# Performance work log

Measured on AMD Instinct MI355X. Metric: run time of the kernel, lower is better.

Reference implementation:

```python
import jax, jax.numpy as jnp
import numpy as np

L, B, D, Di, N, H, P, K, M, V = 4, 8, 2048, 4096, 128, 64, 64, 4, 8, 50288
Cch = Di + 2 * N           # conv channels = 4352
Dout = 2 * Di + 2 * N + H  # in_proj out = 8512
EPS = 1e-5


def _rms(x, w):
    return x * jax.lax.rsqrt(jnp.mean(x * x, axis=-1, keepdims=True) + EPS) * w


def setup_inputs() -> dict:
    key = jax.random.key(0)
    ks = jax.random.split(key, 16)
    s = 0.02
    return {
        "input_ids": jax.random.randint(ks[0], (B, 1), 0, V),
        "emb": jax.random.normal(ks[1], (V, D)) * s,
        "in_proj_w": jax.random.normal(ks[2], (L, D, Dout)) * s,
        "conv_w": jax.random.normal(ks[3], (L, Cch, K)) * s,
        "conv_b": jax.random.normal(ks[4], (L, Cch)) * s,
        "A_log": jax.random.normal(ks[5], (L, H)) * 0.5,
        "dt_bias": jax.random.normal(ks[6], (L, H)) * 0.5,
        "D_param": jax.random.normal(ks[7], (L, H)) * 0.5,
        "mixer_norm_w": jnp.ones((L, Di)),
        "out_proj_w": jax.random.normal(ks[8], (L, Di, D)) * s,
        "layer_norm_w": jnp.ones((L, D)),
        "norm_f_w": jnp.ones((D,)),
        "W_mc": jax.random.normal(ks[9], (L, M + 1)).at[:, -1].set(5.0),
        "conv_state": jax.random.normal(ks[10], (L, B, Cch, K)) * 0.1,
        "ssm_state": jax.random.normal(ks[11], (L, B, H, P, N)) * 0.1,
        "cached_states": jax.random.normal(ks[12], (L, B, M, H, P, N)) * 0.1,
    }


def reference(input_ids, emb, in_proj_w, conv_w, conv_b, A_log, dt_bias, D_param,
              mixer_norm_w, out_proj_w, layer_norm_w, norm_f_w, W_mc,
              conv_state, ssm_state, cached_states):
    ids = input_ids[:, 0]              # (B,)
    res = emb[ids]                     # (B, D) token embedding gather
    for l in range(L):
        xn = _rms(res, layer_norm_w[l])
        zxbcdt = xn @ in_proj_w[l]     # (B, Dout)
        z = zxbcdt[:, :Di]
        xBC = zxbcdt[:, Di:Di + Cch]
        dt = zxbcdt[:, Di + Cch:]
        # circular conv-state shift + depthwise conv over kernel dim
        cs = jnp.concatenate([conv_state[l][:, :, 1:], xBC[:, :, None]], axis=-1)
        xBC = jax.nn.silu(jnp.sum(cs * conv_w[l][None], axis=-1) + conv_b[l])
        x, Bm, Cm = xBC[:, :Di], xBC[:, Di:Di + N], xBC[:, Di + N:]
        dt = jax.nn.softplus(dt + dt_bias[l])                 # (B, H)
        dA = jnp.exp(dt * (-jnp.exp(A_log[l])))               # (B, H)
        x = x.reshape(B, H, P)
        dBx = jnp.einsum('bh,bn,bhp->bhpn', dt, Bm, x)        # (B,H,P,N)
        ssm = ssm_state[l] * dA[:, :, None, None] + dBx       # (B,H,P,N)
        # softmax-weighted fusion of cached segment states + current state
        w = jax.nn.softmax(W_mc[l])                           # (M+1,)
        fused = jnp.einsum('bmhpn,m->bhpn', cached_states[l], w[:-1]) + w[-1] * ssm
        y = jnp.einsum('bhpn,bn->bhp', fused, Cm) + D_param[l][None, :, None] * x
        y = y.reshape(B, Di)
        y = _rms(y * jax.nn.silu(z), mixer_norm_w[l])         # gated RMSNorm
        res = res + y @ out_proj_w[l]
    res = _rms(res, norm_f_w)
    logits = res @ emb.T               # tied lm_head
    return logits[:, None, :]          # (B, 1, V)
```

## Files before the change

### kernel.cpp

```cpp
#include <hip/hip_runtime.h>
#include <hip/hip_bf16.h>
#include <math.h>

#define LN 4
#define B_ 8
#define D_ 2048
#define DI 4096
#define N_ 128
#define H_ 64
#define P_ 64
#define K_ 4
#define M_ 8
#define V_ 50288
#define CCH (DI + 2*N_)
#define DOUT (2*DI + 2*N_ + H_)
#define EPSF 1e-5f
#define KT_IN 32
#define KT_OUT 128
#define SSQS 16

typedef float f32x4 __attribute__((ext_vector_type(4)));

__device__ inline float wave_sum(float v) {
  #pragma unroll
  for (int off = 32; off > 0; off >>= 1) v += __shfl_xor(v, off, 64);
  return v;
}

__device__ inline float fold_reduce8(const float a[8], int lane) {
  float t0[4];
  #pragma unroll
  for (int r = 0; r < 4; ++r) {
    float keep = (lane & 1) ? a[2*r+1] : a[2*r];
    float send = (lane & 1) ? a[2*r]   : a[2*r+1];
    t0[r] = keep + __shfl_xor(send, 1, 64);
  }
  float t1[2];
  #pragma unroll
  for (int r = 0; r < 2; ++r) {
    float keep = (lane & 2) ? t0[2*r+1] : t0[2*r];
    float send = (lane & 2) ? t0[2*r]   : t0[2*r+1];
    t1[r] = keep + __shfl_xor(send, 2, 64);
  }
  float keep = (lane & 4) ? t1[1] : t1[0];
  float send = (lane & 4) ? t1[0] : t1[1];
  float u = keep + __shfl_xor(send, 4, 64);
  u += __shfl_xor(u, 8, 64);
  u += __shfl_xor(u, 16, 64);
  u += __shfl_xor(u, 32, 64);
  return u;
}

__global__ __launch_bounds__(256)
void k_inproj1_first(const int* __restrict__ ids, const float* __restrict__ emb,
                     const float* __restrict__ lnw, const float* __restrict__ W,
                     float* __restrict__ pin) {
  __shared__ float xs[8][64];
  __shared__ float sred[4][8];
  int tid = threadIdx.x, lane = tid & 63, wid = tid >> 6;
  int jt = blockIdx.x % 9, kt = blockIdx.x / 9;
  int k0 = kt * 64;
  float ssq[8];
  #pragma unroll
  for (int r = 0; r < 8; ++r) {
    const float* row = emb + (size_t)ids[r] * D_;
    f32x4 a = *reinterpret_cast<const f32x4*>(row + tid * 8);
    f32x4 c = *reinterpret_cast<const f32x4*>(row + tid * 8 + 4);
    ssq[r] = a[0]*a[0] + a[1]*a[1] + a[2]*a[2] + a[3]*a[3]
           + c[0]*c[0] + c[1]*c[1] + c[2]*c[2] + c[3]*c[3];
  }
  #pragma unroll
  for (int r = 0; r < 8; ++r) {
    float wsum = wave_sum(ssq[r]);
    if (lane == 0) sred[wid][r] = wsum;
  }
  __syncthreads();
  for (int i = tid; i < 8 * 64; i += 256) {
    int r = i >> 6, kk = i & 63;
    const float* row = emb + (size_t)ids[r] * D_;
    float tot = sred[0][r] + sred[1][r] + sred[2][r] + sred[3][r];
    float scale = rsqrtf(tot / (float)D_ + EPSF);
    xs[r][kk] = row[k0 + kk] * scale * lnw[k0 + kk];
  }
  __syncthreads();
  int j = jt * 1024 + tid * 4;
  if (j >= DOUT) return;
  f32x4 acc[8];
  #pragma unroll
  for (int r = 0; r < 8; ++r) acc[r] = (f32x4)0.f;
  const float* Wp = W + (size_t)k0 * DOUT + j;
  for (int kk = 0; kk < 64; ++kk) {
    f32x4 w4 = __builtin_nontemporal_load(
        reinterpret_cast<const f32x4*>(Wp + (size_t)kk * DOUT));
    #pragma unroll
    for (int r = 0; r < 8; ++r) acc[r] += w4 * xs[r][kk];
  }
  #pragma unroll
  for (int r = 0; r < 8; ++r)
    *reinterpret_cast<f32x4*>(&pin[((size_t)kt * 8 + r) * DOUT + j]) = acc[r];
}

__global__ __launch_bounds__(256)
void k_inproj1(const float* __restrict__ res, const float* __restrict__ ssq_in,
               const float* __restrict__ lnw, const float* __restrict__ W,
               float* __restrict__ pin) {
  __shared__ float xs[8][64];
  int tid = threadIdx.x;
  int jt = blockIdx.x % 9, kt = blockIdx.x / 9;
  int k0 = kt * 64;
  for (int i = tid; i < 8 * 64; i += 256) {
    int r = i >> 6, kk = i & 63;
    float scale = rsqrtf(ssq_in[r * SSQS] / (float)D_ + EPSF);
    xs[r][kk] = res[r * D_ + k0 + kk] * scale * lnw[k0 + kk];
  }
  __syncthreads();
  int j = jt * 1024 + tid * 4;
  if (j >= DOUT) return;
  f32x4 acc[8];
  #pragma unroll
  for (int r = 0; r < 8; ++r) acc[r] = (f32x4)0.f;
  const float* Wp = W + (size_t)k0 * DOUT + j;
  for (int kk = 0; kk < 64; ++kk) {
    f32x4 w4 = __builtin_nontemporal_load(
        reinterpret_cast<const f32x4*>(Wp + (size_t)kk * DOUT));
    #pragma unroll
    for (int r = 0; r < 8; ++r) acc[r] += w4 * xs[r][kk];
  }
  #pragma unroll
  for (int r = 0; r < 8; ++r)
    *reinterpret_cast<f32x4*>(&pin[((size_t)kt * 8 + r) * DOUT + j]) = acc[r];
}

__global__ __launch_bounds__(256)
void k_inproj2_conv(const float* __restrict__ pin, const float* __restrict__ conv_state,
                    const float* __restrict__ conv_w, const float* __restrict__ conv_b,
                    const float* __restrict__ A_log, const float* __restrict__ dt_bias,
                    const float* __restrict__ W_mc,
                    float* __restrict__ zx, float* __restrict__ xbc,
                    float* __restrict__ dts, float* __restrict__ dav,
                    float* __restrict__ wmc) {
  __shared__ f32x4 red[4][64];
  const int TOT4 = B_ * DOUT / 4;
  int tid = threadIdx.x;
  int el = tid & 63, kq = tid >> 6;
  int e = blockIdx.x * 64 + el;
  f32x4 s = (f32x4)0.f;
  const f32x4* p4 = reinterpret_cast<const f32x4*>(pin) + e;
  #pragma unroll
  for (int kk = 0; kk < 8; ++kk)
    s += p4[(size_t)(kq * 8 + kk) * TOT4];
  red[kq][el] = s;
  __syncthreads();
  if (tid >= 64) return;
  s = red[0][tid] + red[1][tid] + red[2][tid] + red[3][tid];
  reinterpret_cast<f32x4*>(zx)[e] = s;
  int c4 = e * 4;
  int b = c4 / DOUT;
  int c = c4 - b * DOUT;
  #pragma unroll
  for (int q = 0; q < 4; ++q) {
    int ce = c + q;
    if (ce >= DI && ce < DI + CCH) {
      int cc = ce - DI;
      f32x4 cs4 = *reinterpret_cast<const f32x4*>(conv_state + ((size_t)b * CCH + cc) * K_);
      f32x4 cw4 = *reinterpret_cast<const f32x4*>(conv_w + (size_t)cc * K_);
      float v = cs4[1] * cw4[0] + cs4[2] * cw4[1] + cs4[3] * cw4[2]
              + s[q] * cw4[3] + conv_b[cc];
      xbc[b * CCH + cc] = v / (1.f + expf(-v));
    } else if (ce >= DI + CCH) {
      int h = ce - DI - CCH;
      float x = s[q] + dt_bias[h];
      float sp = (x > 20.f) ? x : log1pf(expf(x));
      dts[b * 64 + h] = sp;
      dav[b * 64 + h] = expf(-expf(A_log[h]) * sp);
    }
  }
  if (blockIdx.x == 0 && tid == 0) {
    float mx = -1e30f;
    for (int i = 0; i < M_ + 1; ++i) mx = fmaxf(mx, W_mc[i]);
    float e2[M_ + 1], sum = 0.f;
    for (int i = 0; i < M_ + 1; ++i) { e2[i] = expf(W_mc[i] - mx); sum += e2[i]; }
    for (int i = 0; i < M_ + 1; ++i) wmc[i] = e2[i] / sum;
  }
}

__global__ __launch_bounds__(256)
void k_state(const float* __restrict__ xbc, const float* __restrict__ dts,
             const float* __restrict__ dav, const float* __restrict__ Dp_,
             const float* __restrict__ wmc, const float* __restrict__ ssm,
             const float* __restrict__ cached, float* __restrict__ y) {
  int wg = blockIdx.x * 4 + (threadIdx.x >> 6);
  int lane = threadIdx.x & 63;
  int b = wg >> 11;
  int h = (wg >> 5) & 63;
  int pp = wg & 31;
  int hf = lane >> 5, il = lane & 31;
  int p = pp * 2 + hf;
  float xv  = xbc[b * CCH + h * 64 + p];
  float dtv = dts[b * 64 + h];
  float da  = dav[b * 64 + h];
  float w8  = wmc[8];
  const f32x4* xb4 = reinterpret_cast<const f32x4*>(xbc);
  f32x4 B4 = xb4[b * (CCH / 4) + DI / 4 + il];
  f32x4 C4 = xb4[b * (CCH / 4) + DI / 4 + N_ / 4 + il];
  const f32x4* sp4 = reinterpret_cast<const f32x4*>(ssm) +
                     ((size_t)((b * H_ + h) * P_ + p)) * (N_ / 4) + il;
  const f32x4* cp4 = reinterpret_cast<const f32x4*>(cached) +
                     ((size_t)(((b * M_) * H_ + h) * P_ + p)) * (N_ / 4) + il;
  f32x4 s4 = __builtin_nontemporal_load(sp4);
  f32x4 f4 = (s4 * da + B4 * (dtv * xv)) * w8;
  #pragma unroll
  for (int m = 0; m < 8; ++m) {
    f32x4 c4 = __builtin_nontemporal_load(cp4 + (size_t)m * (H_ * P_ * N_ / 4));
    f4 += c4 * wmc[m];
  }
  f4 *= C4;
  float acc = f4[0] + f4[1] + f4[2] + f4[3];
  #pragma unroll
  for (int off = 1; off < 32; off <<= 1) acc += __shfl_xor(acc, off, 64);
  if (il == 0) y[b * DI + h * 64 + p] = acc + Dp_[h] * xv;
}

__global__ __launch_bounds__(1024)
void k_gatednorm(const float* __restrict__ y, const float* __restrict__ zx,
                 const float* __restrict__ mnw, float* __restrict__ yg,
                 float* __restrict__ ssq_in) {
  __shared__ float lds[16];
  int b = blockIdx.x, tid = threadIdx.x;
  if (tid < 8) ssq_in[tid * SSQS] = 0.f;
  float tv[4];
  float ss = 0.f;
  #pragma unroll
  for (int t = 0; t < 4; ++t) {
    int i = tid + t * 1024;
    float z = zx[b * DOUT + i];
    float v = y[b * DI + i] * (z / (1.f + expf(-z)));
    tv[t] = v; ss += v * v;
  }
  float wsum = wave_sum(ss);
  int lane = tid & 63, wid = tid >> 6;
  if (lane == 0) lds[wid] = wsum;
  __syncthreads();
  float tot = 0.f;
  #pragma unroll
  for (int i = 0; i < 16; ++i) tot += lds[i];
  float scale = rsqrtf(tot / (float)DI + EPSF);
  #pragma unroll
  for (int t = 0; t < 4; ++t) {
    int i = tid + t * 1024;
    yg[b * DI + i] = tv[t] * scale * mnw[i];
  }
}

__global__ void k_outproj1(const float* __restrict__ yg, const float* __restrict__ W,
                           float* __restrict__ pout) {
  __shared__ float xs[8][32];
  int jt = blockIdx.x & 1, kt = blockIdx.x >> 1;
  int k0 = kt * 32;
  for (int i = threadIdx.x; i < 8 * 32; i += 256) {
    int r = i >> 5, kk = i & 31;
    xs[r][kk] = yg[r * DI + k0 + kk];
  }
  __syncthreads();
  int j = jt * 1024 + threadIdx.x * 4;
  f32x4 acc[8];
  #pragma unroll
  for (int r = 0; r < 8; ++r) acc[r] = (f32x4)0.f;
  const float* Wp = W + (size_t)k0 * D_ + j;
  for (int kk = 0; kk < 32; ++kk) {
    f32x4 w4 = __builtin_nontemporal_load(
        reinterpret_cast<const f32x4*>(Wp + (size_t)kk * D_));
    #pragma unroll
    for (int r = 0; r < 8; ++r) acc[r] += w4 * xs[r][kk];
  }
  #pragma unroll
  for (int r = 0; r < 8; ++r)
    *reinterpret_cast<f32x4*>(&pout[((size_t)kt * 8 + r) * D_ + j]) = acc[r];
}

__global__ __launch_bounds__(256)
void k_outproj2(const float* __restrict__ pout, float* __restrict__ res,
                const int* __restrict__ ids, const float* __restrict__ emb,
                float* __restrict__ ssq_in) {
  __shared__ f32x4 red[16][16];
  const int TOT4 = B_ * D_ / 4;
  int tid = threadIdx.x;
  int pl = tid & 15, kq = tid >> 4;
  int pos = blockIdx.x * 16 + pl;
  const f32x4* p4 = reinterpret_cast<const f32x4*>(pout) + pos;
  f32x4 s = (f32x4)0.f;
  #pragma unroll
  for (int kk = 0; kk < 8; ++kk)
    s += p4[(size_t)(kq * 8 + kk) * TOT4];
  red[pl][kq] = s;
  __syncthreads();
  if (tid < 16) {
    f32x4 tot = (f32x4)0.f;
    #pragma unroll
    for (int q = 0; q < 16; ++q) tot += red[tid][q];
    int mypos = blockIdx.x * 16 + tid;
    f32x4* r4 = reinterpret_cast<f32x4*>(res);
    f32x4 nv;
    if (ids) {
      int b = mypos >> 9, d4 = mypos & 511;
      f32x4 base = reinterpret_cast<const f32x4*>(emb)[(size_t)ids[b] * (D_ / 4) + d4];
      nv = base + tot;
    } else {
      nv = r4[mypos] + tot;
    }
    r4[mypos] = nv;
    float ps = nv[0]*nv[0] + nv[1]*nv[1] + nv[2]*nv[2] + nv[3]*nv[3];
    #pragma unroll
    for (int off = 1; off < 16; off <<= 1) ps += __shfl_xor(ps, off, 64);
    if (tid == 0) atomicAdd(&ssq_in[(mypos >> 9) * SSQS], ps);
  }
}

#define SL_ 4
#define KS_ (D_ / SL_)
#define NVB16 (V_ / 16)
__global__ __launch_bounds__(256)
void k_logits(const float* __restrict__ res, const float* __restrict__ ssq_in,
              const float* __restrict__ nfw, const float* __restrict__ emb,
              float* __restrict__ pl) {
  __shared__ f32x4 xs[8][KS_ / 4];
  int s = blockIdx.x & 3, vb = blockIdx.x >> 2;
  const f32x4* res4 = reinterpret_cast<const f32x4*>(res);
  const f32x4* nfw4 = reinterpret_cast<const f32x4*>(nfw);
  for (int i = threadIdx.x; i < 8 * (KS_ / 4); i += 256) {
    int r = i >> 7, q = i & 127;
    float scale = rsqrtf(ssq_in[r * SSQS] / (float)D_ + EPSF);
    xs[r][q] = res4[r * (D_ / 4) + s * (KS_ / 4) + q] * scale
             * nfw4[s * (KS_ / 4) + q];
  }
  __syncthreads();
  int wid = threadIdx.x >> 6, lane = threadIdx.x & 63;
  int v0 = vb * 16 + wid * 4;
  const f32x4* e4 = reinterpret_cast<const f32x4*>(emb);
  #pragma unroll
  for (int vv = 0; vv < 4; ++vv) {
    int v = v0 + vv;
    const f32x4* ep = e4 + (size_t)v * (D_ / 4) + s * (KS_ / 4);
    float acc[8] = {0,0,0,0,0,0,0,0};
    #pragma unroll
    for (int st = 0; st < KS_ / 256; ++st) {
      int c = st * 64 + lane;
      f32x4 e = __builtin_nontemporal_load(ep + c);
      #pragma unroll
      for (int r = 0; r < 8; ++r) {
        f32x4 x = xs[r][c];
        acc[r] += e[0]*x[0] + e[1]*x[1] + e[2]*x[2] + e[3]*x[3];
      }
    }
    float u = fold_reduce8(acc, lane);
    if (lane < 8) pl[((size_t)s * 8 + lane) * V_ + v] = u;
  }
}

__global__ __launch_bounds__(256)
void k_logits2(const float* __restrict__ pl, float* __restrict__ out) {
  int v = blockIdx.x * 256 + threadIdx.x;
  if (v >= V_) return;
  int r = blockIdx.y;
  float t = pl[(size_t)r * V_ + v]
          + pl[((size_t)8  + r) * V_ + v]
          + pl[((size_t)16 + r) * V_ + v]
          + pl[((size_t)24 + r) * V_ + v];
  out[(size_t)r * V_ + v] = t;
}

extern "C" void kernel_launch(void* const* d_in, const int* in_sizes, int n_in,
                              void* d_out, int out_size, void* d_ws, size_t ws_size,
                              hipStream_t stream) {
  const int*   ids    = (const int*)  d_in[0];
  const float* emb    = (const float*)d_in[1];
  const float* inW    = (const float*)d_in[2];
  const float* convW  = (const float*)d_in[3];
  const float* convB  = (const float*)d_in[4];
  const float* Alog   = (const float*)d_in[5];
  const float* dtB    = (const float*)d_in[6];
  const float* Dpar   = (const float*)d_in[7];
  const float* mnw    = (const float*)d_in[8];
  const float* outW   = (const float*)d_in[9];
  const float* lnw    = (const float*)d_in[10];
  const float* nfw    = (const float*)d_in[11];
  const float* Wmc    = (const float*)d_in[12];
  const float* convS  = (const float*)d_in[13];
  const float* ssmS   = (const float*)d_in[14];
  const float* cached = (const float*)d_in[15];
  float* out = (float*)d_out;
  float* ws  = (float*)d_ws;

  float* res   = ws;
  float* zx    = ws + 16384;
  float* xbc   = ws + 84480;
  float* dts   = ws + 119296;
  float* dav   = ws + 119808;
  float* wmc   = ws + 120320;
  float* ssqi  = ws + 120384;
  float* y     = ws + 120512;
  float* yg    = ws + 153280;
  float* pin   = ws + 186048;
  float* pout  = ws + 2365120;
  float* pl    = ws + 4462272;

  for (int l = 0; l < LN; ++l) {
    if (l == 0)
      k_inproj1_first<<<288, 256, 0, stream>>>(ids, emb, lnw, inW, pin);
    else
      k_inproj1<<<288, 256, 0, stream>>>(res, ssqi, lnw + (size_t)l * D_,
                                         inW + (size_t)l * D_ * DOUT, pin);
    k_inproj2_conv<<<266, 256, 0, stream>>>(pin,
        convS + (size_t)l * B_ * CCH * K_, convW + (size_t)l * CCH * K_,
        convB + (size_t)l * CCH, Alog + l * H_, dtB + l * H_, Wmc + l * (M_ + 1),
        zx, xbc, dts, dav, wmc);
    k_state<<<4096, 256, 0, stream>>>(xbc, dts, dav, Dpar + l * H_, wmc,
        ssmS + (size_t)l * B_ * H_ * P_ * N_,
        cached + (size_t)l * B_ * M_ * H_ * P_ * N_, y);
    k_gatednorm<<<8, 1024, 0, stream>>>(y, zx, mnw + (size_t)l * DI, yg, ssqi);
    k_outproj1<<<256, 256, 0, stream>>>(yg, outW + (size_t)l * DI * D_, pout);
    k_outproj2<<<256, 256, 0, stream>>>(pout, res,
                                        (l == 0) ? ids : nullptr, emb, ssqi);
  }
  k_logits<<<NVB16 * SL_, 256, 0, stream>>>(res, ssqi, nfw, emb, pl);
  k_logits2<<<dim3((V_ + 255) / 256, 8), 256, 0, stream>>>(pl, out);
}
```

Measured before the change: 418.6 us.

## Fuse gated RMSNorm into state and out-projection kernels, drop gatednorm launch

Removes the separate k_gatednorm kernel (8 blocks of 1024 threads) by having k_state emit per-block partial sums of the squared gated output, and having k_outproj1 reduce those partials and apply the gate, scale and norm weight while staging its input tile. The ssq_in zeroing moves into k_inproj2_conv. This saves one launch and a low-parallelism kernel per layer. In exchange, every out-projection block re-reduces 4096 partials and recomputes the silu gate, and k_state gains a block-level syncthreads.

```diff
diff --git a/kernel.cpp b/kernel.cpp
--- a/kernel.cpp
+++ b/kernel.cpp
@@ -138,10 +138,11 @@
                     const float* __restrict__ W_mc,
                     float* __restrict__ zx, float* __restrict__ xbc,
                     float* __restrict__ dts, float* __restrict__ dav,
-                    float* __restrict__ wmc) {
+                    float* __restrict__ wmc, float* __restrict__ ssq_in) {
   __shared__ f32x4 red[4][64];
   const int TOT4 = B_ * DOUT / 4;
   int tid = threadIdx.x;
+  if (blockIdx.x == 1 && tid < 8) ssq_in[tid * SSQS] = 0.f;
   int el = tid & 63, kq = tid >> 6;
   int e = blockIdx.x * 64 + el;
   f32x4 s = (f32x4)0.f;
@@ -185,10 +186,12 @@
 }
 
 __global__ __launch_bounds__(256)
-void k_state(const float* __restrict__ xbc, const float* __restrict__ dts,
-             const float* __restrict__ dav, const float* __restrict__ Dp_,
-             const float* __restrict__ wmc, const float* __restrict__ ssm,
-             const float* __restrict__ cached, float* __restrict__ y) {
+void k_state(const float* __restrict__ xbc, const float* __restrict__ zx,
+             const float* __restrict__ dts, const float* __restrict__ dav,
+             const float* __restrict__ Dp_, const float* __restrict__ wmc,
+             const float* __restrict__ ssm, const float* __restrict__ cached,
+             float* __restrict__ y, float* __restrict__ gpart) {
+  __shared__ float gred[8];
   int wg = blockIdx.x * 4 + (threadIdx.x >> 6);
   int lane = threadIdx.x & 63;
   int b = wg >> 11;
@@ -218,51 +221,49 @@
   float acc = f4[0] + f4[1] + f4[2] + f4[3];
   #pragma unroll
   for (int off = 1; off < 32; off <<= 1) acc += __shfl_xor(acc, off, 64);
-  if (il == 0) y[b * DI + h * 64 + p] = acc + Dp_[h] * xv;
-}
-
-__global__ __launch_bounds__(1024)
-void k_gatednorm(const float* __restrict__ y, const float* __restrict__ zx,
-                 const float* __restrict__ mnw, float* __restrict__ yg,
-                 float* __restrict__ ssq_in) {
-  __shared__ float lds[16];
-  int b = blockIdx.x, tid = threadIdx.x;
-  if (tid < 8) ssq_in[tid * SSQS] = 0.f;
-  float tv[4];
-  float ss = 0.f;
-  #pragma unroll
-  for (int t = 0; t < 4; ++t) {
-    int i = tid + t * 1024;
-    float z = zx[b * DOUT + i];
-    float v = y[b * DI + i] * (z / (1.f + expf(-z)));
-    tv[t] = v; ss += v * v;
-  }
-  float wsum = wave_sum(ss);
-  int lane = tid & 63, wid = tid >> 6;
-  if (lane == 0) lds[wid] = wsum;
-  __syncthreads();
-  float tot = 0.f;
-  #pragma unroll
-  for (int i = 0; i < 16; ++i) tot += lds[i];
-  float scale = rsqrtf(tot / (float)DI + EPSF);
-  #pragma unroll
-  for (int t = 0; t < 4; ++t) {
-    int i = tid + t * 1024;
-    yg[b * DI + i] = tv[t] * scale * mnw[i];
-  }
-}
-
-__global__ void k_outproj1(const float* __restrict__ yg, const float* __restrict__ W,
-                           float* __restrict__ pout) {
+  if (il == 0) {
+    float yv = acc + Dp_[h] * xv;
+    int d = h * 64 + p;
+    y[b * DI + d] = yv;
+    float z = zx[b * DOUT + d];
+    float v = yv * (z / (1.f + expf(-z)));
+    gred[(threadIdx.x >> 6) * 2 + hf] = v * v;
+  }
+  __syncthreads();
+  if (threadIdx.x == 0) {
+    gpart[blockIdx.x] = gred[0] + gred[1] + gred[2] + gred[3]
+                      + gred[4] + gred[5] + gred[6] + gred[7];
+  }
+}
+
+__global__ __launch_bounds__(256)
+void k_outproj1(const float* __restrict__ y, const float* __restrict__ zx,
+                const float* __restrict__ mnw, const float* __restrict__ gpart,
+                const float* __restrict__ W, float* __restrict__ pout) {
   __shared__ float xs[8][32];
+  __shared__ float sred[8];
+  int tid = threadIdx.x;
+  {
+    int r = tid >> 5, t32 = tid & 31;
+    const f32x4* g4 = reinterpret_cast<const f32x4*>(gpart) + r * 128 + t32 * 4;
+    f32x4 a = g4[0] + g4[1] + g4[2] + g4[3];
+    float s = a[0] + a[1] + a[2] + a[3];
+    #pragma unroll
+    for (int off = 1; off < 32; off <<= 1) s += __shfl_xor(s, off, 64);
+    if (t32 == 0) sred[r] = s;
+  }
+  __syncthreads();
   int jt = blockIdx.x & 1, kt = blockIdx.x >> 1;
   int k0 = kt * 32;
-  for (int i = threadIdx.x; i < 8 * 32; i += 256) {
-    int r = i >> 5, kk = i & 31;
-    xs[r][kk] = yg[r * DI + k0 + kk];
-  }
-  __syncthreads();
-  int j = jt * 1024 + threadIdx.x * 4;
+  {
+    int r = tid >> 5, kk = tid & 31;
+    float scale = rsqrtf(sred[r] / (float)DI + EPSF);
+    float z = zx[r * DOUT + k0 + kk];
+    float g = z / (1.f + expf(-z));
+    xs[r][kk] = y[r * DI + k0 + kk] * g * scale * mnw[k0 + kk];
+  }
+  __syncthreads();
+  int j = jt * 1024 + tid * 4;
   f32x4 acc[8];
   #pragma unroll
   for (int r = 0; r < 8; ++r) acc[r] = (f32x4)0.f;
@@ -398,11 +399,11 @@
   float* dav   = ws + 119808;
   float* wmc   = ws + 120320;
   float* ssqi  = ws + 120384;
-  float* y     = ws + 120512;
-  float* yg    = ws + 153280;
-  float* pin   = ws + 186048;
-  float* pout  = ws + 2365120;
-  float* pl    = ws + 4462272;
+  float* gpart = ws + 120512;
+  float* y     = ws + 124608;
+  float* pin   = ws + 157376;
+  float* pout  = ws + 2336448;
+  float* pl    = ws + 4433600;
 
   for (int l = 0; l < LN; ++l) {
     if (l == 0)
@@ -413,12 +414,12 @@
     k_inproj2_conv<<<266, 256, 0, stream>>>(pin,
         convS + (size_t)l * B_ * CCH * K_, convW + (size_t)l * CCH * K_,
         convB + (size_t)l * CCH, Alog + l * H_, dtB + l * H_, Wmc + l * (M_ + 1),
-        zx, xbc, dts, dav, wmc);
-    k_state<<<4096, 256, 0, stream>>>(xbc, dts, dav, Dpar + l * H_, wmc,
+        zx, xbc, dts, dav, wmc, ssqi);
+    k_state<<<4096, 256, 0, stream>>>(xbc, zx, dts, dav, Dpar + l * H_, wmc,
         ssmS + (size_t)l * B_ * H_ * P_ * N_,
-        cached + (size_t)l * B_ * M_ * H_ * P_ * N_, y);
-    k_gatednorm<<<8, 1024, 0, stream>>>(y, zx, mnw + (size_t)l * DI, yg, ssqi);
-    k_outproj1<<<256, 256, 0, stream>>>(yg, outW + (size_t)l * DI * D_, pout);
+        cached + (size_t)l * B_ * M_ * H_ * P_ * N_, y, gpart);
+    k_outproj1<<<256, 256, 0, stream>>>(y, zx, mnw + (size_t)l * DI, gpart,
+                                        outW + (size_t)l * DI * D_, pout);
     k_outproj2<<<256, 256, 0, stream>>>(pout, res,
                                         (l == 0) ? ids : nullptr, emb, ssqi);
   }
```

New measurement: 410.6 us. About the same (-1.9%).
